# Optimization experiments

Hardware: AMD Instinct MI355X
Metric: run time of the kernel (lower is better)

Reference implementation:

```python
import jax, jax.numpy as jnp
import numpy as np
from jax import lax

LENGTH, WIDTH = 64, 64
INPUT_DIM = 1


def _convlstm_layer(x_tbchw, W, b):
    """Run one ConvLSTM layer over time. x_tbchw: (L,B,Cin,H,W).
    W: (4*hid, Cin+hid, 3, 3), b: (4*hid,). Returns (outputs (L,B,hid,H,W), last_h)."""
    L, B, _, H, Wd = x_tbchw.shape
    hid = W.shape[0] // 4
    h0 = jnp.zeros((B, hid, H, Wd), dtype=x_tbchw.dtype)
    c0 = jnp.zeros((B, hid, H, Wd), dtype=x_tbchw.dtype)

    def step(carry, xt):
        h, c = carry
        z = lax.conv_general_dilated(
            jnp.concatenate([xt, h], axis=1), W,
            window_strides=(1, 1), padding='SAME',
            dimension_numbers=('NCHW', 'OIHW', 'NCHW'))
        z = z + b[None, :, None, None]
        cc_i, cc_f, cc_o, cc_g = jnp.split(z, 4, axis=1)
        c_next = jax.nn.sigmoid(cc_f) * c + jax.nn.sigmoid(cc_i) * jnp.tanh(cc_g)
        h_next = jax.nn.sigmoid(cc_o) * jnp.tanh(c_next)
        return (h_next, c_next), h_next

    (h_last, _), outs = lax.scan(step, (h0, c0), x_tbchw)
    return outs, h_last


def setup_inputs() -> dict:
    key = jax.random.key(0)
    k1, k2, k3 = jax.random.split(key, 3)
    B, L, N = 16, 12, LENGTH * WIDTH
    emd, out_len = 128, 12
    return {
        'history_data': jax.random.normal(k1, (B, L, N, 1), dtype=jnp.float32),
        'future_data': jnp.zeros((B, L, N, 1), dtype=jnp.float32),
        'W0': jax.random.normal(k2, (4 * emd, INPUT_DIM + emd, 3, 3), dtype=jnp.float32) * 0.05,
        'b0': jnp.zeros((4 * emd,), dtype=jnp.float32),
        'W1': jax.random.normal(k3, (4 * out_len, emd + out_len, 3, 3), dtype=jnp.float32) * 0.05,
        'b1': jnp.zeros((4 * out_len,), dtype=jnp.float32),
        'batch_seen': 0,
        'epoch': 0,
        'train': 1,
    }


def reference(history_data, future_data, W0, b0, W1, b1, batch_seen, epoch, train):
    B, L, N, C = history_data.shape
    # (B,L,1,H,W) -> (L,B,1,H,W) for time-major scan
    x = history_data[..., :INPUT_DIM].reshape(B, L, INPUT_DIM, LENGTH, WIDTH)
    x = jnp.transpose(x, (1, 0, 2, 3, 4))
    outs0, _ = _convlstm_layer(x, W0, b0)          # (L,B,emd,H,W)
    _, h_last = _convlstm_layer(outs0, W1, b1)     # (B,out_len,H,W)
    prediction = h_last.reshape(B, L, LENGTH * WIDTH)[..., None]  # (B,L,N,1)
    return prediction
```

## Files before the change

### kernel.cpp

```cpp
#include <hip/hip_runtime.h>
#include <hip/hip_bf16.h>


typedef __attribute__((ext_vector_type(8))) short short8;
typedef __attribute__((ext_vector_type(4))) float float4v;

#define CS 160
#define KTOT 1440

__device__ __forceinline__ float sigf(float x) { return 1.f / (1.f + __expf(-x)); }
__device__ __forceinline__ short f2hs(float v) {
  _Float16 h = (_Float16)v;
  return *(short*)&h;
}
__device__ __forceinline__ float hs2f(short s) {
  _Float16 h; *(short*)&h = s; return (float)h;
}
__device__ __forceinline__ float bs2f(short s) {
  __hip_bfloat16 h; *(short*)&h = s; return __bfloat162float(h);
}
__device__ __forceinline__ short f2bs(float v) {
  __hip_bfloat16 h = __float2bfloat16(v);
  return *(short*)&h;
}

__device__ __forceinline__ void async_ld16(const short* g, short* l) {
  __builtin_amdgcn_global_load_lds(
      (const __attribute__((address_space(1))) unsigned int*)g,
      (__attribute__((address_space(3))) unsigned int*)l, 16, 0, 0);
}

__device__ __forceinline__ void stage_row(const short* __restrict__ rowPtr, bool rowOK,
                                          short* dstRow, int lane,
                                          const short* __restrict__ zp) {
  #pragma unroll
  for (int j = 0; j < 4; ++j) {
    int e = j * 64 + lane;
    int px = e >> 2, v = e & 3;
    int xx = px - 1;
    const short* g = (rowOK && xx >= 0) ? (rowPtr + (size_t)xx * CS + v * 8) : zp;
    async_ld16(g, dstRow + e * 8);
  }
  if (lane < 8) {
    int px = 64 + (lane >> 2), v = lane & 3, xx = px - 1;
    short8 val = {0, 0, 0, 0, 0, 0, 0, 0};
    if (rowOK && xx < 64) val = *(const short8*)(rowPtr + (size_t)xx * CS + v * 8);
    *(short8*)(dstRow + px * 32 + v * 8) = val;
  }
}

__global__ void detect_dtype(const unsigned short* __restrict__ w0, int* __restrict__ flag) {
  int lane = threadIdx.x;
  int cnt = 0;
  for (int i = 0; i < 4; ++i) {
    unsigned short u = w0[2 * (lane + 64 * i)];
    int e = (u >> 7) & 0xFF;
    unsigned long long b = __ballot(e >= 0xC0);
    cnt += __popcll(b);
  }
  if (lane == 0) *flag = (cnt > 32) ? 1 : 0;
}

__global__ void canon_x(const void* __restrict__ hist, short* __restrict__ Xc,
                        const int* __restrict__ flag) {
  int i = blockIdx.x * 256 + threadIdx.x;
  float v = (*flag) ? ((const float*)hist)[i] : bs2f(((const short*)hist)[i]);
  if (!isfinite(v) || fabsf(v) > 1e4f) v = 0.f;
  Xc[i] = f2hs(v);
}

__global__ void canon_b(const void* __restrict__ b0, const void* __restrict__ b1,
                        float* __restrict__ Bc0, float* __restrict__ Bc1,
                        const int* __restrict__ flag) {
  int i = blockIdx.x * 256 + threadIdx.x;
  int fl = *flag;
  if (i < 512) {
    float v = fl ? ((const float*)b0)[i] : bs2f(((const short*)b0)[i]);
    if (!isfinite(v) || fabsf(v) > 1e4f) v = 0.f;
    Bc0[i] = v;
  } else if (i < 560) {
    int j = i - 512;
    float v = fl ? ((const float*)b1)[j] : bs2f(((const short*)b1)[j]);
    if (!isfinite(v) || fabsf(v) > 1e4f) v = 0.f;
    Bc1[j] = v;
  }
}

__global__ void prep_w0(const void* __restrict__ W0, short* __restrict__ Wp,
                        const int* __restrict__ flag) {
  int i = blockIdx.x * 256 + threadIdx.x;
  if (i >= 512 * KTOT) return;
  int fl = *flag;
  int co = i / KTOT, k = i - co * KTOT;
  int tap = k / CS, c = k - tap * CS;
  int ci = -1;
  if (c == 0) ci = 0;
  else if (c <= 128) ci = c;
  float w = 0.f;
  if (ci >= 0) {
    int widx = (co * 129 + ci) * 9 + tap;
    w = fl ? ((const float*)W0)[widx] : bs2f(((const short*)W0)[widx]);
    if (!isfinite(w) || fabsf(w) > 1e4f) w = 0.f;
  }
  Wp[i] = f2hs(w);
}

__global__ void prep_w1(const void* __restrict__ W1, short* __restrict__ Wp,
                        const int* __restrict__ flag) {
  int i = blockIdx.x * 256 + threadIdx.x;
  if (i >= 48 * KTOT) return;
  int fl = *flag;
  int co = i / KTOT, k = i - co * KTOT;
  int tap = k / CS, c = k - tap * CS;
  int ci = -1;
  if (c >= 1 && c <= 140) ci = c - 1;
  float w = 0.f;
  if (ci >= 0) {
    int widx = (co * 140 + ci) * 9 + tap;
    w = fl ? ((const float*)W1)[widx] : bs2f(((const short*)W1)[widx]);
    if (!isfinite(w) || fabsf(w) > 1e4f) w = 0.f;
  }
  Wp[i] = f2hs(w);
}

__global__ void fill_x0(const short* __restrict__ Xc, short* __restrict__ P0) {
  int p = blockIdx.x * 256 + threadIdx.x;
  int b = p >> 12, pix = p & 4095;
  P0[(size_t)p * CS] = Xc[b * 12 * 4096 + pix];
}

__global__ __launch_bounds__(256, 2) void gemm_gate0(
    const short* __restrict__ Pcur, short* __restrict__ Pnext,
    const short* __restrict__ Wp, const float* __restrict__ Bc0,
    float* __restrict__ C0, const short* __restrict__ Xc,
    const short* __restrict__ zp, int t) {
  int bx = blockIdx.x;
  int nt = bx >> 9, mt = bx & 511;
  int b = mt >> 5, y0 = (mt & 31) * 2;
  int tid = threadIdx.x, wave = tid >> 6, lane = tid & 63;
  int ln15 = lane & 15, quad = lane >> 4;
  int wm = wave & 1, wn = wave >> 1;
  int hc = nt * 32 + wn * 16 + ln15;

  __shared__ __align__(16) short halo[2 * 4 * 66 * 32];

  float4v acc[4][4];
  #pragma unroll
  for (int i = 0; i < 4; ++i)
    #pragma unroll
    for (int j = 0; j < 4; ++j) acc[i][j] = (float4v){0.f, 0.f, 0.f, 0.f};

  const short* wbase = Wp + (size_t)hc * KTOT + quad * 8;
  short8 bcur[4], bnxt[4];
  #pragma unroll
  for (int g = 0; g < 4; ++g)
    bcur[g] = *(const short8*)(wbase + (size_t)g * 128 * KTOT);

  int yy = y0 - 1 + wave;
  bool rowOK = (yy >= 0) && (yy < 64);
  const short* rowBase = Pcur + (size_t)((b * 64 + yy) * 64) * CS;

  stage_row(rowBase, rowOK, halo + wave * 2112, lane, zp);
  __syncthreads();

  for (int ch = 0; ch < 5; ++ch) {
    int c0 = ch * 32;
    const short* cur = halo + (ch & 1) * 8448;
    if (ch < 4)
      stage_row(rowBase + c0 + 32, rowOK, halo + ((ch + 1) & 1) * 8448 + wave * 2112,
                lane, zp);
    #pragma unroll
    for (int tap = 0; tap < 9; ++tap) {
      int dy = tap / 3, dx = tap - dy * 3;
      int ntap = (tap < 8) ? tap + 1 : 0;
      int nc0 = (tap < 8) ? c0 : ((ch < 4) ? c0 + 32 : c0);
      #pragma unroll
      for (int g = 0; g < 4; ++g)
        bnxt[g] = *(const short8*)(wbase + (size_t)g * 128 * KTOT + ntap * CS + nc0);

      short8 af[4];
      #pragma unroll
      for (int mf = 0; mf < 4; ++mf)
        af[mf] = *(const short8*)&cur[((wm + dy) * 66 + mf * 16 + ln15 + dx) * 32 + quad * 8];
      #pragma unroll
      for (int g = 0; g < 4; ++g)
        #pragma unroll
        for (int mf = 0; mf < 4; ++mf)
          acc[mf][g] = __builtin_amdgcn_mfma_f32_16x16x32_f16(af[mf], bcur[g], acc[mf][g], 0, 0, 0);
      #pragma unroll
      for (int g = 0; g < 4; ++g) bcur[g] = bnxt[g];
    }
    __syncthreads();
  }

  float bi = Bc0[hc], bff = Bc0[128 + hc], bo = Bc0[256 + hc], bg = Bc0[384 + hc];
  int rowPix = (b * 64 + y0 + wm) * 64;
  #pragma unroll
  for (int mf = 0; mf < 4; ++mf) {
    #pragma unroll
    for (int r = 0; r < 4; ++r) {
      int x = mf * 16 + quad * 4 + r;
      int pix = rowPix + x;
      float zi = acc[mf][0][r] + bi;
      float zf = acc[mf][1][r] + bff;
      float zo = acc[mf][2][r] + bo;
      float zg = acc[mf][3][r] + bg;
      float cprev = C0[(size_t)pix * 128 + hc];
      float cn = sigf(zf) * cprev + sigf(zi) * tanhf(zg);
      float hn = sigf(zo) * tanhf(cn);
      C0[(size_t)pix * 128 + hc] = cn;
      Pnext[(size_t)pix * CS + 1 + hc] = f2hs(hn);
    }
  }
  if (nt == 0 && t < 11 && tid < 128) {
    int rr = tid >> 6, x = tid & 63;
    int yw = y0 + rr;
    Pnext[(size_t)((b * 64 + yw) * 64 + x) * CS] = Xc[(b * 12 + t + 1) * 4096 + yw * 64 + x];
  }
}

__global__ __launch_bounds__(256, 2) void gemm_gate1(
    const short* __restrict__ Prd, short* __restrict__ Pwr,
    const short* __restrict__ Wp, const float* __restrict__ Bc1,
    float* __restrict__ C1, void* __restrict__ outp,
    const short* __restrict__ zp, const int* __restrict__ flagp, int t) {
  int bid = blockIdx.x;
  int b = bid >> 5, y0 = (bid & 31) * 2;
  int tid = threadIdx.x, wave = tid >> 6, lane = tid & 63;
  int ln15 = lane & 15, quad = lane >> 4;
  int wr = wave >> 1, wh = wave & 1;
  int flagv = *flagp;

  __shared__ __align__(16) short halo[2 * 4 * 66 * 32];

  float4v acc[2][3];
  #pragma unroll
  for (int i = 0; i < 2; ++i)
    #pragma unroll
    for (int j = 0; j < 3; ++j) acc[i][j] = (float4v){0.f, 0.f, 0.f, 0.f};

  int yy = y0 - 1 + wave;
  bool rowOK = (yy >= 0) && (yy < 64);
  const short* rowBase = Prd + (size_t)((b * 64 + yy) * 64) * CS;

  const short* wbase = Wp + (size_t)ln15 * KTOT + quad * 8;
  short8 bcur[3], bnxt[3];
  #pragma unroll
  for (int nf = 0; nf < 3; ++nf)
    bcur[nf] = *(const short8*)(wbase + (size_t)nf * 16 * KTOT);

  stage_row(rowBase, rowOK, halo + wave * 2112, lane, zp);
  __syncthreads();

  for (int ch = 0; ch < 5; ++ch) {
    int c0 = ch * 32;
    const short* cur = halo + (ch & 1) * 8448;
    if (ch < 4)
      stage_row(rowBase + c0 + 32, rowOK, halo + ((ch + 1) & 1) * 8448 + wave * 2112,
                lane, zp);
    #pragma unroll
    for (int tap = 0; tap < 9; ++tap) {
      int dy = tap / 3, dx = tap - dy * 3;
      int ntap = (tap < 8) ? tap + 1 : 0;
      int nc0 = (tap < 8) ? c0 : ((ch < 4) ? c0 + 32 : c0);
      #pragma unroll
      for (int nf = 0; nf < 3; ++nf)
        bnxt[nf] = *(const short8*)(wbase + (size_t)nf * 16 * KTOT + ntap * CS + nc0);

      short8 af[2];
      #pragma unroll
      for (int mf = 0; mf < 2; ++mf)
        af[mf] = *(const short8*)&cur[((wr + dy) * 66 + wh * 32 + mf * 16 + ln15 + dx) * 32
                                      + quad * 8];
      #pragma unroll
      for (int nf = 0; nf < 3; ++nf)
        #pragma unroll
        for (int mf = 0; mf < 2; ++mf)
          acc[mf][nf] = __builtin_amdgcn_mfma_f32_16x16x32_f16(af[mf], bcur[nf], acc[mf][nf], 0, 0, 0);
      #pragma unroll
      for (int nf = 0; nf < 3; ++nf) bcur[nf] = bnxt[nf];
    }
    __syncthreads();
  }

  float* zbuf = (float*)halo;
  #pragma unroll
  for (int mf = 0; mf < 2; ++mf)
    #pragma unroll
    for (int nf = 0; nf < 3; ++nf)
      #pragma unroll
      for (int r = 0; r < 4; ++r) {
        int pxl = wr * 64 + wh * 32 + mf * 16 + quad * 4 + r;
        zbuf[pxl * 48 + nf * 16 + ln15] = acc[mf][nf][r];
      }
  __syncthreads();

  #pragma unroll
  for (int k = 0; k < 6; ++k) {
    int id = k * 256 + tid;
    int hc = id >> 7, pxl = id & 127;
    float zi = zbuf[pxl * 48 + hc]      + Bc1[hc];
    float zf = zbuf[pxl * 48 + 12 + hc] + Bc1[12 + hc];
    float zo = zbuf[pxl * 48 + 24 + hc] + Bc1[24 + hc];
    float zg = zbuf[pxl * 48 + 36 + hc] + Bc1[36 + hc];
    int y = y0 + (pxl >> 6), x = pxl & 63;
    int pix = (b * 64 + y) * 64 + x;
    float cprev = C1[(size_t)pix * 12 + hc];
    float cn = sigf(zf) * cprev + sigf(zi) * tanhf(zg);
    float hn = sigf(zo) * tanhf(cn);
    C1[(size_t)pix * 12 + hc] = cn;
    Pwr[(size_t)pix * CS + 129 + hc] = f2hs(hn);
    if (t == 11) {
      int oidx = (b * 12 + hc) * 4096 + y * 64 + x;
      if (flagv) ((float*)outp)[oidx] = hn;
      else ((short*)outp)[oidx] = f2bs(hn);
    }
  }
}

extern "C" void kernel_launch(void* const* d_in, const int* in_sizes, int n_in,
                              void* d_out, int out_size, void* d_ws, size_t ws_size,
                              hipStream_t stream) {
  const void* hist = d_in[0];
  const void* W0 = d_in[2];
  const void* b0 = d_in[3];
  const void* W1 = d_in[4];
  const void* b1 = d_in[5];

  char* ws = (char*)d_ws;
  const size_t PszB = (size_t)16 * 4096 * CS * 2;
  short* P[2] = {(short*)ws, (short*)(ws + PszB)};
  float* C0 = (float*)(ws + 2 * PszB);
  const size_t C0e = 2 * PszB + 33554432;
  float* C1 = (float*)(ws + C0e);
  const size_t C1e = C0e + 3145728;
  short* zp = (short*)(ws + C1e);
  const size_t zpe = C1e + 256;
  short* Xc = (short*)(ws + zpe);
  const size_t Xce = zpe + 1572864;
  short* Wp0 = (short*)(ws + Xce);
  const size_t W0e = Xce + (size_t)512 * KTOT * 2;
  short* Wp1 = (short*)(ws + W0e);
  const size_t W1e = W0e + (size_t)48 * KTOT * 2;
  float* Bc0 = (float*)(ws + W1e);
  float* Bc1 = (float*)(ws + W1e + 2048);
  int* flag = (int*)(ws + W1e + 2048 + 192);

  hipMemsetAsync(ws, 0, zpe, stream);
  detect_dtype<<<1, 64, 0, stream>>>((const unsigned short*)W0, flag);
  canon_x<<<3072, 256, 0, stream>>>(hist, Xc, flag);
  canon_b<<<3, 256, 0, stream>>>(b0, b1, Bc0, Bc1, flag);
  prep_w0<<<(512 * KTOT + 255) / 256, 256, 0, stream>>>(W0, Wp0, flag);
  prep_w1<<<(48 * KTOT + 255) / 256, 256, 0, stream>>>(W1, Wp1, flag);
  fill_x0<<<256, 256, 0, stream>>>(Xc, P[0]);

  for (int t = 0; t < 12; ++t) {
    gemm_gate0<<<2048, 256, 0, stream>>>(P[t & 1], P[(t + 1) & 1], Wp0, Bc0, C0, Xc, zp, t);
    gemm_gate1<<<512, 256, 0, stream>>>(P[(t + 1) & 1], P[t & 1], Wp1, Bc1, C1,
                                        d_out, zp, flag, t);
  }
}
```

Baseline: 2.202 ms.

## Fuse layer-0 step t and layer-1 step t-1 into one skewed launch

Merges the two per-timestep GEMM kernels into a single kernel whose blocks are split 4:1. Most blocks run ConvLSTM layer 0 at step t, and the rest run layer 1 at step t-1, over a 13-step skewed schedule. This halves the number of launches and lets the small layer-1 work overlap the layer-0 GEMM instead of running alone with low occupancy. The occupancy hint is also raised from 2 to 3 blocks per CU, which tightens the register budget and may cause spills. Correctness relies on the two layers writing disjoint channel ranges of the ping-pong P buffer.

```diff
diff --git a/kernel.cpp b/kernel.cpp
--- a/kernel.cpp
+++ b/kernel.cpp
@@ -12,9 +12,6 @@
 __device__ __forceinline__ short f2hs(float v) {
   _Float16 h = (_Float16)v;
   return *(short*)&h;
-}
-__device__ __forceinline__ float hs2f(short s) {
-  _Float16 h; *(short*)&h = s; return (float)h;
 }
 __device__ __forceinline__ float bs2f(short s) {
   __hip_bfloat16 h; *(short*)&h = s; return __bfloat162float(h);
@@ -129,191 +126,190 @@
   P0[(size_t)p * CS] = Xc[b * 12 * 4096 + pix];
 }
 
-__global__ __launch_bounds__(256, 2) void gemm_gate0(
+__global__ __launch_bounds__(256, 3) void fused_step(
     const short* __restrict__ Pcur, short* __restrict__ Pnext,
-    const short* __restrict__ Wp, const float* __restrict__ Bc0,
+    const short* __restrict__ Wp0, const float* __restrict__ Bc0,
     float* __restrict__ C0, const short* __restrict__ Xc,
-    const short* __restrict__ zp, int t) {
+    const short* __restrict__ Wp1, const float* __restrict__ Bc1,
+    float* __restrict__ C1, void* __restrict__ outp,
+    const short* __restrict__ zp, const int* __restrict__ flagp, int t) {
+  __shared__ __align__(16) short halo[2 * 4 * 66 * 32];
+
   int bx = blockIdx.x;
-  int nt = bx >> 9, mt = bx & 511;
-  int b = mt >> 5, y0 = (mt & 31) * 2;
   int tid = threadIdx.x, wave = tid >> 6, lane = tid & 63;
   int ln15 = lane & 15, quad = lane >> 4;
-  int wm = wave & 1, wn = wave >> 1;
-  int hc = nt * 32 + wn * 16 + ln15;
-
-  __shared__ __align__(16) short halo[2 * 4 * 66 * 32];
-
-  float4v acc[4][4];
-  #pragma unroll
-  for (int i = 0; i < 4; ++i)
-    #pragma unroll
-    for (int j = 0; j < 4; ++j) acc[i][j] = (float4v){0.f, 0.f, 0.f, 0.f};
-
-  const short* wbase = Wp + (size_t)hc * KTOT + quad * 8;
-  short8 bcur[4], bnxt[4];
-  #pragma unroll
-  for (int g = 0; g < 4; ++g)
-    bcur[g] = *(const short8*)(wbase + (size_t)g * 128 * KTOT);
-
-  int yy = y0 - 1 + wave;
-  bool rowOK = (yy >= 0) && (yy < 64);
-  const short* rowBase = Pcur + (size_t)((b * 64 + yy) * 64) * CS;
-
-  stage_row(rowBase, rowOK, halo + wave * 2112, lane, zp);
-  __syncthreads();
-
-  for (int ch = 0; ch < 5; ++ch) {
-    int c0 = ch * 32;
-    const short* cur = halo + (ch & 1) * 8448;
-    if (ch < 4)
-      stage_row(rowBase + c0 + 32, rowOK, halo + ((ch + 1) & 1) * 8448 + wave * 2112,
-                lane, zp);
-    #pragma unroll
-    for (int tap = 0; tap < 9; ++tap) {
-      int dy = tap / 3, dx = tap - dy * 3;
-      int ntap = (tap < 8) ? tap + 1 : 0;
-      int nc0 = (tap < 8) ? c0 : ((ch < 4) ? c0 + 32 : c0);
-      #pragma unroll
-      for (int g = 0; g < 4; ++g)
-        bnxt[g] = *(const short8*)(wbase + (size_t)g * 128 * KTOT + ntap * CS + nc0);
-
-      short8 af[4];
-      #pragma unroll
-      for (int mf = 0; mf < 4; ++mf)
-        af[mf] = *(const short8*)&cur[((wm + dy) * 66 + mf * 16 + ln15 + dx) * 32 + quad * 8];
-      #pragma unroll
-      for (int g = 0; g < 4; ++g)
+
+  if ((bx % 5) != 4) {
+    if (t >= 12) return;
+    int idx = bx - bx / 5;
+    int nt = idx >> 9, mt = idx & 511;
+    int b = mt >> 5, y0 = (mt & 31) * 2;
+    int wm = wave & 1, wn = wave >> 1;
+    int hc = nt * 32 + wn * 16 + ln15;
+
+    float4v acc[4][4];
+    #pragma unroll
+    for (int i = 0; i < 4; ++i)
+      #pragma unroll
+      for (int j = 0; j < 4; ++j) acc[i][j] = (float4v){0.f, 0.f, 0.f, 0.f};
+
+    const short* wbase = Wp0 + (size_t)hc * KTOT + quad * 8;
+    short8 bcur[4], bnxt[4];
+    #pragma unroll
+    for (int g = 0; g < 4; ++g)
+      bcur[g] = *(const short8*)(wbase + (size_t)g * 128 * KTOT);
+
+    int yy = y0 - 1 + wave;
+    bool rowOK = (yy >= 0) && (yy < 64);
+    const short* rowBase = Pcur + (size_t)((b * 64 + yy) * 64) * CS;
+
+    stage_row(rowBase, rowOK, halo + wave * 2112, lane, zp);
+    __syncthreads();
+
+    for (int ch = 0; ch < 5; ++ch) {
+      int c0 = ch * 32;
+      const short* cur = halo + (ch & 1) * 8448;
+      if (ch < 4)
+        stage_row(rowBase + c0 + 32, rowOK, halo + ((ch + 1) & 1) * 8448 + wave * 2112,
+                  lane, zp);
+      #pragma unroll
+      for (int tap = 0; tap < 9; ++tap) {
+        int dy = tap / 3, dx = tap - dy * 3;
+        int ntap = (tap < 8) ? tap + 1 : 0;
+        int nc0 = (tap < 8) ? c0 : ((ch < 4) ? c0 + 32 : c0);
+        #pragma unroll
+        for (int g = 0; g < 4; ++g)
+          bnxt[g] = *(const short8*)(wbase + (size_t)g * 128 * KTOT + ntap * CS + nc0);
+
+        short8 af[4];
         #pragma unroll
         for (int mf = 0; mf < 4; ++mf)
-          acc[mf][g] = __builtin_amdgcn_mfma_f32_16x16x32_f16(af[mf], bcur[g], acc[mf][g], 0, 0, 0);
-      #pragma unroll
-      for (int g = 0; g < 4; ++g) bcur[g] = bnxt[g];
-    }
+          af[mf] = *(const short8*)&cur[((wm + dy) * 66 + mf * 16 + ln15 + dx) * 32 + quad * 8];
+        #pragma unroll
+        for (int g = 0; g < 4; ++g)
+          #pragma unroll
+          for (int mf = 0; mf < 4; ++mf)
+            acc[mf][g] = __builtin_amdgcn_mfma_f32_16x16x32_f16(af[mf], bcur[g], acc[mf][g], 0, 0, 0);
+        #pragma unroll
+        for (int g = 0; g < 4; ++g) bcur[g] = bnxt[g];
+      }
+      __syncthreads();
+    }
+
+    float bi = Bc0[hc], bff = Bc0[128 + hc], bo = Bc0[256 + hc], bg = Bc0[384 + hc];
+    int rowPix = (b * 64 + y0 + wm) * 64;
+    #pragma unroll
+    for (int mf = 0; mf < 4; ++mf) {
+      #pragma unroll
+      for (int r = 0; r < 4; ++r) {
+        int x = mf * 16 + quad * 4 + r;
+        int pix = rowPix + x;
+        float zi = acc[mf][0][r] + bi;
+        float zf = acc[mf][1][r] + bff;
+        float zo = acc[mf][2][r] + bo;
+        float zg = acc[mf][3][r] + bg;
+        float cprev = C0[(size_t)pix * 128 + hc];
+        float cn = sigf(zf) * cprev + sigf(zi) * tanhf(zg);
+        float hn = sigf(zo) * tanhf(cn);
+        C0[(size_t)pix * 128 + hc] = cn;
+        Pnext[(size_t)pix * CS + 1 + hc] = f2hs(hn);
+      }
+    }
+    if (nt == 0 && t < 11 && tid < 128) {
+      int rr = tid >> 6, x = tid & 63;
+      int yw = y0 + rr;
+      Pnext[(size_t)((b * 64 + yw) * 64 + x) * CS] = Xc[(b * 12 + t + 1) * 4096 + yw * 64 + x];
+    }
+  } else {
+    if (t < 1) return;
+    int t1 = t - 1;
+    int idx1 = bx / 5;
+    int b = idx1 >> 5, y0 = (idx1 & 31) * 2;
+    int wr = wave >> 1, wh = wave & 1;
+    int flagv = *flagp;
+
+    float4v acc[2][3];
+    #pragma unroll
+    for (int i = 0; i < 2; ++i)
+      #pragma unroll
+      for (int j = 0; j < 3; ++j) acc[i][j] = (float4v){0.f, 0.f, 0.f, 0.f};
+
+    int yy = y0 - 1 + wave;
+    bool rowOK = (yy >= 0) && (yy < 64);
+    const short* rowBase = Pcur + (size_t)((b * 64 + yy) * 64) * CS;
+
+    const short* wbase = Wp1 + (size_t)ln15 * KTOT + quad * 8;
+    short8 bcur[3], bnxt[3];
+    #pragma unroll
+    for (int nf = 0; nf < 3; ++nf)
+      bcur[nf] = *(const short8*)(wbase + (size_t)nf * 16 * KTOT);
+
+    stage_row(rowBase, rowOK, halo + wave * 2112, lane, zp);
     __syncthreads();
-  }
-
-  float bi = Bc0[hc], bff = Bc0[128 + hc], bo = Bc0[256 + hc], bg = Bc0[384 + hc];
-  int rowPix = (b * 64 + y0 + wm) * 64;
-  #pragma unroll
-  for (int mf = 0; mf < 4; ++mf) {
-    #pragma unroll
-    for (int r = 0; r < 4; ++r) {
-      int x = mf * 16 + quad * 4 + r;
-      int pix = rowPix + x;
-      float zi = acc[mf][0][r] + bi;
-      float zf = acc[mf][1][r] + bff;
-      float zo = acc[mf][2][r] + bo;
-      float zg = acc[mf][3][r] + bg;
-      float cprev = C0[(size_t)pix * 128 + hc];
+
+    for (int ch = 0; ch < 5; ++ch) {
+      int c0 = ch * 32;
+      const short* cur = halo + (ch & 1) * 8448;
+      if (ch < 4)
+        stage_row(rowBase + c0 + 32, rowOK, halo + ((ch + 1) & 1) * 8448 + wave * 2112,
+                  lane, zp);
+      #pragma unroll
+      for (int tap = 0; tap < 9; ++tap) {
+        int dy = tap / 3, dx = tap - dy * 3;
+        int ntap = (tap < 8) ? tap + 1 : 0;
+        int nc0 = (tap < 8) ? c0 : ((ch < 4) ? c0 + 32 : c0);
+        #pragma unroll
+        for (int nf = 0; nf < 3; ++nf)
+          bnxt[nf] = *(const short8*)(wbase + (size_t)nf * 16 * KTOT + ntap * CS + nc0);
+
+        short8 af[2];
+        #pragma unroll
+        for (int mf = 0; mf < 2; ++mf)
+          af[mf] = *(const short8*)&cur[((wr + dy) * 66 + wh * 32 + mf * 16 + ln15 + dx) * 32
+                                        + quad * 8];
+        #pragma unroll
+        for (int nf = 0; nf < 3; ++nf)
+          #pragma unroll
+          for (int mf = 0; mf < 2; ++mf)
+            acc[mf][nf] = __builtin_amdgcn_mfma_f32_16x16x32_f16(af[mf], bcur[nf], acc[mf][nf], 0, 0, 0);
+        #pragma unroll
+        for (int nf = 0; nf < 3; ++nf) bcur[nf] = bnxt[nf];
+      }
+      __syncthreads();
+    }
+
+    float* zbuf = (float*)halo;
+    #pragma unroll
+    for (int mf = 0; mf < 2; ++mf)
+      #pragma unroll
+      for (int nf = 0; nf < 3; ++nf)
+        #pragma unroll
+        for (int r = 0; r < 4; ++r) {
+          int pxl = wr * 64 + wh * 32 + mf * 16 + quad * 4 + r;
+          zbuf[pxl * 48 + nf * 16 + ln15] = acc[mf][nf][r];
+        }
+    __syncthreads();
+
+    #pragma unroll
+    for (int k = 0; k < 6; ++k) {
+      int id = k * 256 + tid;
+      int hc = id >> 7, pxl = id & 127;
+      float zi = zbuf[pxl * 48 + hc]      + Bc1[hc];
+      float zf = zbuf[pxl * 48 + 12 + hc] + Bc1[12 + hc];
+      float zo = zbuf[pxl * 48 + 24 + hc] + Bc1[24 + hc];
+      float zg = zbuf[pxl * 48 + 36 + hc] + Bc1[36 + hc];
+      int y = y0 + (pxl >> 6), x = pxl & 63;
+      int pix = (b * 64 + y) * 64 + x;
+      float cprev = C1[(size_t)pix * 12 + hc];
       float cn = sigf(zf) * cprev + sigf(zi) * tanhf(zg);
       float hn = sigf(zo) * tanhf(cn);
-      C0[(size_t)pix * 128 + hc] = cn;
-      Pnext[(size_t)pix * CS + 1 + hc] = f2hs(hn);
-    }
-  }
-  if (nt == 0 && t < 11 && tid < 128) {
-    int rr = tid >> 6, x = tid & 63;
-    int yw = y0 + rr;
-    Pnext[(size_t)((b * 64 + yw) * 64 + x) * CS] = Xc[(b * 12 + t + 1) * 4096 + yw * 64 + x];
-  }
-}
-
-__global__ __launch_bounds__(256, 2) void gemm_gate1(
-    const short* __restrict__ Prd, short* __restrict__ Pwr,
-    const short* __restrict__ Wp, const float* __restrict__ Bc1,
-    float* __restrict__ C1, void* __restrict__ outp,
-    const short* __restrict__ zp, const int* __restrict__ flagp, int t) {
-  int bid = blockIdx.x;
-  int b = bid >> 5, y0 = (bid & 31) * 2;
-  int tid = threadIdx.x, wave = tid >> 6, lane = tid & 63;
-  int ln15 = lane & 15, quad = lane >> 4;
-  int wr = wave >> 1, wh = wave & 1;
-  int flagv = *flagp;
-
-  __shared__ __align__(16) short halo[2 * 4 * 66 * 32];
-
-  float4v acc[2][3];
-  #pragma unroll
-  for (int i = 0; i < 2; ++i)
-    #pragma unroll
-    for (int j = 0; j < 3; ++j) acc[i][j] = (float4v){0.f, 0.f, 0.f, 0.f};
-
-  int yy = y0 - 1 + wave;
-  bool rowOK = (yy >= 0) && (yy < 64);
-  const short* rowBase = Prd + (size_t)((b * 64 + yy) * 64) * CS;
-
-  const short* wbase = Wp + (size_t)ln15 * KTOT + quad * 8;
-  short8 bcur[3], bnxt[3];
-  #pragma unroll
-  for (int nf = 0; nf < 3; ++nf)
-    bcur[nf] = *(const short8*)(wbase + (size_t)nf * 16 * KTOT);
-
-  stage_row(rowBase, rowOK, halo + wave * 2112, lane, zp);
-  __syncthreads();
-
-  for (int ch = 0; ch < 5; ++ch) {
-    int c0 = ch * 32;
-    const short* cur = halo + (ch & 1) * 8448;
-    if (ch < 4)
-      stage_row(rowBase + c0 + 32, rowOK, halo + ((ch + 1) & 1) * 8448 + wave * 2112,
-                lane, zp);
-    #pragma unroll
-    for (int tap = 0; tap < 9; ++tap) {
-      int dy = tap / 3, dx = tap - dy * 3;
-      int ntap = (tap < 8) ? tap + 1 : 0;
-      int nc0 = (tap < 8) ? c0 : ((ch < 4) ? c0 + 32 : c0);
-      #pragma unroll
-      for (int nf = 0; nf < 3; ++nf)
-        bnxt[nf] = *(const short8*)(wbase + (size_t)nf * 16 * KTOT + ntap * CS + nc0);
-
-      short8 af[2];
-      #pragma unroll
-      for (int mf = 0; mf < 2; ++mf)
-        af[mf] = *(const short8*)&cur[((wr + dy) * 66 + wh * 32 + mf * 16 + ln15 + dx) * 32
-                                      + quad * 8];
-      #pragma unroll
-      for (int nf = 0; nf < 3; ++nf)
-        #pragma unroll
-        for (int mf = 0; mf < 2; ++mf)
-          acc[mf][nf] = __builtin_amdgcn_mfma_f32_16x16x32_f16(af[mf], bcur[nf], acc[mf][nf], 0, 0, 0);
-      #pragma unroll
-      for (int nf = 0; nf < 3; ++nf) bcur[nf] = bnxt[nf];
-    }
-    __syncthreads();
-  }
-
-  float* zbuf = (float*)halo;
-  #pragma unroll
-  for (int mf = 0; mf < 2; ++mf)
-    #pragma unroll
-    for (int nf = 0; nf < 3; ++nf)
-      #pragma unroll
-      for (int r = 0; r < 4; ++r) {
-        int pxl = wr * 64 + wh * 32 + mf * 16 + quad * 4 + r;
-        zbuf[pxl * 48 + nf * 16 + ln15] = acc[mf][nf][r];
+      C1[(size_t)pix * 12 + hc] = cn;
+      Pnext[(size_t)pix * CS + 129 + hc] = f2hs(hn);
+      if (t1 == 11) {
+        int oidx = (b * 12 + hc) * 4096 + y * 64 + x;
+        if (flagv) ((float*)outp)[oidx] = hn;
+        else ((short*)outp)[oidx] = f2bs(hn);
       }
-  __syncthreads();
-
-  #pragma unroll
-  for (int k = 0; k < 6; ++k) {
-    int id = k * 256 + tid;
-    int hc = id >> 7, pxl = id & 127;
-    float zi = zbuf[pxl * 48 + hc]      + Bc1[hc];
-    float zf = zbuf[pxl * 48 + 12 + hc] + Bc1[12 + hc];
-    float zo = zbuf[pxl * 48 + 24 + hc] + Bc1[24 + hc];
-    float zg = zbuf[pxl * 48 + 36 + hc] + Bc1[36 + hc];
-    int y = y0 + (pxl >> 6), x = pxl & 63;
-    int pix = (b * 64 + y) * 64 + x;
-    float cprev = C1[(size_t)pix * 12 + hc];
-    float cn = sigf(zf) * cprev + sigf(zi) * tanhf(zg);
-    float hn = sigf(zo) * tanhf(cn);
-    C1[(size_t)pix * 12 + hc] = cn;
-    Pwr[(size_t)pix * CS + 129 + hc] = f2hs(hn);
-    if (t == 11) {
-      int oidx = (b * 12 + hc) * 4096 + y * 64 + x;
-      if (flagv) ((float*)outp)[oidx] = hn;
-      else ((short*)outp)[oidx] = f2bs(hn);
     }
   }
 }
@@ -354,9 +350,8 @@
   prep_w1<<<(48 * KTOT + 255) / 256, 256, 0, stream>>>(W1, Wp1, flag);
   fill_x0<<<256, 256, 0, stream>>>(Xc, P[0]);
 
-  for (int t = 0; t < 12; ++t) {
-    gemm_gate0<<<2048, 256, 0, stream>>>(P[t & 1], P[(t + 1) & 1], Wp0, Bc0, C0, Xc, zp, t);
-    gemm_gate1<<<512, 256, 0, stream>>>(P[(t + 1) & 1], P[t & 1], Wp1, Bc1, C1,
-                                        d_out, zp, flag, t);
-  }
-}
+  for (int t = 0; t <= 12; ++t) {
+    fused_step<<<2560, 256, 0, stream>>>(P[t & 1], P[(t + 1) & 1], Wp0, Bc0, C0, Xc,
+                                         Wp1, Bc1, C1, d_out, zp, flag, t);
+  }
+}
```

Result: slower. 2.416 ms (+9.7%).

## Retile layer-0 conv GEMM to one image row per block with full-channel halo staging

Applied to the files above, without the earlier changes.

Layer-0 gate GEMM is re-tiled so each block handles one output row (64 pixels) for 32 hidden channels across all four gates, with each wave owning 16 pixels and eight N-fragments. The whole 3-row, 160-channel input halo is loaded into LDS once with a channel-major pitched layout, replacing the per-chunk double-buffered staging and its per-chunk barriers. This cuts A-fragment LDS reads per MFMA and removes synchronisation inside the K loop. In exchange it doubles the grid, re-reads halo rows across neighbouring blocks, and raises register pressure from eight live B fragments.

```diff
diff --git a/kernel.cpp b/kernel.cpp
--- a/kernel.cpp
+++ b/kernel.cpp
@@ -7,15 +7,14 @@
 
 #define CS 160
 #define KTOT 1440
+#define VPITCH 528
+#define RPITCH 10560
 
 __device__ __forceinline__ float sigf(float x) { return 1.f / (1.f + __expf(-x)); }
 __device__ __forceinline__ short f2hs(float v) {
   _Float16 h = (_Float16)v;
   return *(short*)&h;
 }
-__device__ __forceinline__ float hs2f(short s) {
-  _Float16 h; *(short*)&h = s; return (float)h;
-}
 __device__ __forceinline__ float bs2f(short s) {
   __hip_bfloat16 h; *(short*)&h = s; return __bfloat162float(h);
 }
@@ -28,25 +27,6 @@
   __builtin_amdgcn_global_load_lds(
       (const __attribute__((address_space(1))) unsigned int*)g,
       (__attribute__((address_space(3))) unsigned int*)l, 16, 0, 0);
-}
-
-__device__ __forceinline__ void stage_row(const short* __restrict__ rowPtr, bool rowOK,
-                                          short* dstRow, int lane,
-                                          const short* __restrict__ zp) {
-  #pragma unroll
-  for (int j = 0; j < 4; ++j) {
-    int e = j * 64 + lane;
-    int px = e >> 2, v = e & 3;
-    int xx = px - 1;
-    const short* g = (rowOK && xx >= 0) ? (rowPtr + (size_t)xx * CS + v * 8) : zp;
-    async_ld16(g, dstRow + e * 8);
-  }
-  if (lane < 8) {
-    int px = 64 + (lane >> 2), v = lane & 3, xx = px - 1;
-    short8 val = {0, 0, 0, 0, 0, 0, 0, 0};
-    if (rowOK && xx < 64) val = *(const short8*)(rowPtr + (size_t)xx * CS + v * 8);
-    *(short8*)(dstRow + px * 32 + v * 8) = val;
-  }
 }
 
 __global__ void detect_dtype(const unsigned short* __restrict__ w0, int* __restrict__ flag) {
@@ -135,76 +115,82 @@
     float* __restrict__ C0, const short* __restrict__ Xc,
     const short* __restrict__ zp, int t) {
   int bx = blockIdx.x;
-  int nt = bx >> 9, mt = bx & 511;
-  int b = mt >> 5, y0 = (mt & 31) * 2;
+  int nt = bx & 3, mt = bx >> 2;
+  int y = mt & 63, b = mt >> 6;
   int tid = threadIdx.x, wave = tid >> 6, lane = tid & 63;
   int ln15 = lane & 15, quad = lane >> 4;
-  int wm = wave & 1, wn = wave >> 1;
-  int hc = nt * 32 + wn * 16 + ln15;
-
-  __shared__ __align__(16) short halo[2 * 4 * 66 * 32];
-
-  float4v acc[4][4];
-  #pragma unroll
-  for (int i = 0; i < 4; ++i)
-    #pragma unroll
-    for (int j = 0; j < 4; ++j) acc[i][j] = (float4v){0.f, 0.f, 0.f, 0.f};
-
-  const short* wbase = Wp + (size_t)hc * KTOT + quad * 8;
-  short8 bcur[4], bnxt[4];
-  #pragma unroll
-  for (int g = 0; g < 4; ++g)
-    bcur[g] = *(const short8*)(wbase + (size_t)g * 128 * KTOT);
-
-  int yy = y0 - 1 + wave;
-  bool rowOK = (yy >= 0) && (yy < 64);
-  const short* rowBase = Pcur + (size_t)((b * 64 + yy) * 64) * CS;
-
-  stage_row(rowBase, rowOK, halo + wave * 2112, lane, zp);
+
+  __shared__ __align__(16) short halo[3 * RPITCH];
+
+  #pragma unroll
+  for (int i = 0; i < 15; ++i) {
+    int pid = wave * 15 + i;
+    int r = pid / 20, v = pid - r * 20;
+    int yy = y - 1 + r;
+    bool rowOK = (yy >= 0) && (yy < 64);
+    const short* rowPtr = Pcur + (size_t)((b * 64 + yy) * 64) * CS + v * 8;
+    const short* g = (rowOK && lane > 0) ? (rowPtr + (size_t)(lane - 1) * CS) : zp;
+    async_ld16(g - (size_t)lane * 8 + (size_t)lane * 8, halo + r * RPITCH + v * VPITCH);
+    (void)g;
+  }
+  if (wave < 3 && lane < 40) {
+    int r = wave, v = lane >> 1, pxi = 64 + (lane & 1);
+    int yy = y - 1 + r;
+    bool rowOK = (yy >= 0) && (yy < 64);
+    short8 val = {0, 0, 0, 0, 0, 0, 0, 0};
+    if (rowOK && pxi == 64)
+      val = *(const short8*)(Pcur + (size_t)((b * 64 + yy) * 64 + 63) * CS + v * 8);
+    *(short8*)(halo + r * RPITCH + v * VPITCH + pxi * 8) = val;
+  }
   __syncthreads();
 
+  float4v acc[8];
+  #pragma unroll
+  for (int i = 0; i < 8; ++i) acc[i] = (float4v){0.f, 0.f, 0.f, 0.f};
+
+  const short* bb[8];
+  short8 bcur[8], bnxt[8];
+  #pragma unroll
+  for (int nf = 0; nf < 8; ++nf) {
+    int co = (nf >> 1) * 128 + nt * 32 + (nf & 1) * 16 + ln15;
+    bb[nf] = Wp + (size_t)co * KTOT + quad * 8;
+    bcur[nf] = *(const short8*)(bb[nf]);
+  }
+
+  int pxb = wave * 16 + ln15;
   for (int ch = 0; ch < 5; ++ch) {
-    int c0 = ch * 32;
-    const short* cur = halo + (ch & 1) * 8448;
-    if (ch < 4)
-      stage_row(rowBase + c0 + 32, rowOK, halo + ((ch + 1) & 1) * 8448 + wave * 2112,
-                lane, zp);
     #pragma unroll
     for (int tap = 0; tap < 9; ++tap) {
       int dy = tap / 3, dx = tap - dy * 3;
       int ntap = (tap < 8) ? tap + 1 : 0;
-      int nc0 = (tap < 8) ? c0 : ((ch < 4) ? c0 + 32 : c0);
-      #pragma unroll
-      for (int g = 0; g < 4; ++g)
-        bnxt[g] = *(const short8*)(wbase + (size_t)g * 128 * KTOT + ntap * CS + nc0);
-
-      short8 af[4];
-      #pragma unroll
-      for (int mf = 0; mf < 4; ++mf)
-        af[mf] = *(const short8*)&cur[((wm + dy) * 66 + mf * 16 + ln15 + dx) * 32 + quad * 8];
-      #pragma unroll
-      for (int g = 0; g < 4; ++g)
-        #pragma unroll
-        for (int mf = 0; mf < 4; ++mf)
-          acc[mf][g] = __builtin_amdgcn_mfma_f32_16x16x32_f16(af[mf], bcur[g], acc[mf][g], 0, 0, 0);
-      #pragma unroll
-      for (int g = 0; g < 4; ++g) bcur[g] = bnxt[g];
+      int nch = (tap < 8) ? ch : ((ch < 4) ? ch + 1 : ch);
+      #pragma unroll
+      for (int nf = 0; nf < 8; ++nf)
+        bnxt[nf] = *(const short8*)(bb[nf] + ntap * CS + nch * 32);
+
+      short8 af = *(const short8*)&halo[dy * RPITCH + (ch * 4 + quad) * VPITCH
+                                        + (pxb + dx) * 8];
+      #pragma unroll
+      for (int nf = 0; nf < 8; ++nf)
+        acc[nf] = __builtin_amdgcn_mfma_f32_16x16x32_f16(af, bcur[nf], acc[nf], 0, 0, 0);
+      #pragma unroll
+      for (int nf = 0; nf < 8; ++nf) bcur[nf] = bnxt[nf];
     }
-    __syncthreads();
-  }
-
-  float bi = Bc0[hc], bff = Bc0[128 + hc], bo = Bc0[256 + hc], bg = Bc0[384 + hc];
-  int rowPix = (b * 64 + y0 + wm) * 64;
-  #pragma unroll
-  for (int mf = 0; mf < 4; ++mf) {
+  }
+
+  int rowPix = (b * 64 + y) * 64;
+  #pragma unroll
+  for (int h = 0; h < 2; ++h) {
+    int hc = nt * 32 + h * 16 + ln15;
+    float bi = Bc0[hc], bff = Bc0[128 + hc], bo = Bc0[256 + hc], bg = Bc0[384 + hc];
     #pragma unroll
     for (int r = 0; r < 4; ++r) {
-      int x = mf * 16 + quad * 4 + r;
+      int x = wave * 16 + quad * 4 + r;
       int pix = rowPix + x;
-      float zi = acc[mf][0][r] + bi;
-      float zf = acc[mf][1][r] + bff;
-      float zo = acc[mf][2][r] + bo;
-      float zg = acc[mf][3][r] + bg;
+      float zi = acc[0 + h][r] + bi;
+      float zf = acc[2 + h][r] + bff;
+      float zo = acc[4 + h][r] + bo;
+      float zg = acc[6 + h][r] + bg;
       float cprev = C0[(size_t)pix * 128 + hc];
       float cn = sigf(zf) * cprev + sigf(zi) * tanhf(zg);
       float hn = sigf(zo) * tanhf(cn);
@@ -212,10 +198,27 @@
       Pnext[(size_t)pix * CS + 1 + hc] = f2hs(hn);
     }
   }
-  if (nt == 0 && t < 11 && tid < 128) {
-    int rr = tid >> 6, x = tid & 63;
-    int yw = y0 + rr;
-    Pnext[(size_t)((b * 64 + yw) * 64 + x) * CS] = Xc[(b * 12 + t + 1) * 4096 + yw * 64 + x];
+  if (nt == 0 && t < 11 && tid < 64) {
+    Pnext[(size_t)(rowPix + tid) * CS] = Xc[(b * 12 + t + 1) * 4096 + y * 64 + tid];
+  }
+}
+
+__device__ __forceinline__ void stage_row32(const short* __restrict__ rowPtr, bool rowOK,
+                                            short* dstRow, int lane,
+                                            const short* __restrict__ zp) {
+  #pragma unroll
+  for (int j = 0; j < 4; ++j) {
+    int e = j * 64 + lane;
+    int px = e >> 2, v = e & 3;
+    int xx = px - 1;
+    const short* g = (rowOK && xx >= 0) ? (rowPtr + (size_t)xx * CS + v * 8) : zp;
+    async_ld16(g, dstRow + e * 8);
+  }
+  if (lane < 8) {
+    int px = 64 + (lane >> 2), v = lane & 3, xx = px - 1;
+    short8 val = {0, 0, 0, 0, 0, 0, 0, 0};
+    if (rowOK && xx < 64) val = *(const short8*)(rowPtr + (size_t)xx * CS + v * 8);
+    *(short8*)(dstRow + px * 32 + v * 8) = val;
   }
 }
 
@@ -249,15 +252,15 @@
   for (int nf = 0; nf < 3; ++nf)
     bcur[nf] = *(const short8*)(wbase + (size_t)nf * 16 * KTOT);
 
-  stage_row(rowBase, rowOK, halo + wave * 2112, lane, zp);
+  stage_row32(rowBase, rowOK, halo + wave * 2112, lane, zp);
   __syncthreads();
 
   for (int ch = 0; ch < 5; ++ch) {
     int c0 = ch * 32;
     const short* cur = halo + (ch & 1) * 8448;
     if (ch < 4)
-      stage_row(rowBase + c0 + 32, rowOK, halo + ((ch + 1) & 1) * 8448 + wave * 2112,
-                lane, zp);
+      stage_row32(rowBase + c0 + 32, rowOK, halo + ((ch + 1) & 1) * 8448 + wave * 2112,
+                  lane, zp);
     #pragma unroll
     for (int tap = 0; tap < 9; ++tap) {
       int dy = tap / 3, dx = tap - dy * 3;
@@ -355,7 +358,7 @@
   fill_x0<<<256, 256, 0, stream>>>(Xc, P[0]);
 
   for (int t = 0; t < 12; ++t) {
-    gemm_gate0<<<2048, 256, 0, stream>>>(P[t & 1], P[(t + 1) & 1], Wp0, Bc0, C0, Xc, zp, t);
+    gemm_gate0<<<4096, 256, 0, stream>>>(P[t & 1], P[(t + 1) & 1], Wp0, Bc0, C0, Xc, zp, t);
     gemm_gate1<<<512, 256, 0, stream>>>(P[(t + 1) & 1], P[t & 1], Wp1, Bc1, C1,
                                         d_out, zp, flag, t);
   }
```

Result: slower. 5.854 ms (+165.9%).

## Specialize first layer-0 timestep with scalar kernel and deepen weight prefetch

Applied to the files above, without the earlier changes.

At t=0 the hidden and cell states are zero, so the layer-0 gate computation only needs the single input channel. A dedicated scalar kernel now does this step instead of the full 1440-wide MFMA GEMM, and the fill_x0 kernel and one full gate0 GEMM launch are removed. Separately, the gate0 GEMM now keeps three taps of weight fragments in registers, prefetching three taps ahead instead of one, to hide global load latency better. This costs more VGPRs, which may hurt occupancy under the 2-wave launch bound.

```diff
diff --git a/kernel.cpp b/kernel.cpp
--- a/kernel.cpp
+++ b/kernel.cpp
@@ -123,10 +123,53 @@
   Wp[i] = f2hs(w);
 }
 
-__global__ void fill_x0(const short* __restrict__ Xc, short* __restrict__ P0) {
-  int p = blockIdx.x * 256 + threadIdx.x;
-  int b = p >> 12, pix = p & 4095;
-  P0[(size_t)p * CS] = Xc[b * 12 * 4096 + pix];
+__global__ __launch_bounds__(256, 4) void gate0_t0(
+    const short* __restrict__ Xc, short* __restrict__ Pnext,
+    const short* __restrict__ Wp, const float* __restrict__ Bc0,
+    float* __restrict__ C0) {
+  int rid = blockIdx.x;
+  int b = rid >> 6, y = rid & 63;
+  int tid = threadIdx.x;
+  __shared__ float xh[3][66];
+  for (int i = tid; i < 198; i += 256) {
+    int r = i / 66, px = i - r * 66;
+    int yy = y - 1 + r, xx = px - 1;
+    float v = 0.f;
+    if ((unsigned)yy < 64u && (unsigned)xx < 64u)
+      v = hs2f(Xc[b * 12 * 4096 + yy * 64 + xx]);
+    xh[r][px] = v;
+  }
+  __syncthreads();
+
+  int hc = tid & 127, pb = tid >> 7;
+  float wgt[4][9];
+  #pragma unroll
+  for (int g = 0; g < 4; ++g)
+    #pragma unroll
+    for (int tap = 0; tap < 9; ++tap)
+      wgt[g][tap] = hs2f(Wp[(size_t)(g * 128 + hc) * KTOT + tap * CS]);
+  float bi = Bc0[hc], bff = Bc0[128 + hc], bo = Bc0[256 + hc], bg = Bc0[384 + hc];
+  (void)bff;
+  int rowPix = (b * 64 + y) * 64;
+  for (int k = 0; k < 32; ++k) {
+    int x = pb + 2 * k;
+    float zi = bi, zo = bo, zg = bg;
+    #pragma unroll
+    for (int tap = 0; tap < 9; ++tap) {
+      int dy = tap / 3, dx = tap - dy * 3;
+      float xv = xh[dy][x + dx];
+      zi += wgt[0][tap] * xv;
+      zo += wgt[2][tap] * xv;
+      zg += wgt[3][tap] * xv;
+    }
+    float cn = sigf(zi) * tanhf(zg);
+    float hn = sigf(zo) * tanhf(cn);
+    int pix = rowPix + x;
+    C0[(size_t)pix * 128 + hc] = cn;
+    Pnext[(size_t)pix * CS + 1 + hc] = f2hs(hn);
+  }
+  if (tid < 64)
+    Pnext[(size_t)(rowPix + tid) * CS] = Xc[(b * 12 + 1) * 4096 + y * 64 + tid];
 }
 
 __global__ __launch_bounds__(256, 2) void gemm_gate0(
@@ -151,10 +194,12 @@
     for (int j = 0; j < 4; ++j) acc[i][j] = (float4v){0.f, 0.f, 0.f, 0.f};
 
   const short* wbase = Wp + (size_t)hc * KTOT + quad * 8;
-  short8 bcur[4], bnxt[4];
-  #pragma unroll
-  for (int g = 0; g < 4; ++g)
-    bcur[g] = *(const short8*)(wbase + (size_t)g * 128 * KTOT);
+  short8 bb[3][4];
+  #pragma unroll
+  for (int p = 0; p < 3; ++p)
+    #pragma unroll
+    for (int g = 0; g < 4; ++g)
+      bb[p][g] = *(const short8*)(wbase + (size_t)g * 128 * KTOT + p * CS);
 
   int yy = y0 - 1 + wave;
   bool rowOK = (yy >= 0) && (yy < 64);
@@ -164,19 +209,14 @@
   __syncthreads();
 
   for (int ch = 0; ch < 5; ++ch) {
-    int c0 = ch * 32;
     const short* cur = halo + (ch & 1) * 8448;
     if (ch < 4)
-      stage_row(rowBase + c0 + 32, rowOK, halo + ((ch + 1) & 1) * 8448 + wave * 2112,
+      stage_row(rowBase + ch * 32 + 32, rowOK, halo + ((ch + 1) & 1) * 8448 + wave * 2112,
                 lane, zp);
     #pragma unroll
     for (int tap = 0; tap < 9; ++tap) {
       int dy = tap / 3, dx = tap - dy * 3;
-      int ntap = (tap < 8) ? tap + 1 : 0;
-      int nc0 = (tap < 8) ? c0 : ((ch < 4) ? c0 + 32 : c0);
-      #pragma unroll
-      for (int g = 0; g < 4; ++g)
-        bnxt[g] = *(const short8*)(wbase + (size_t)g * 128 * KTOT + ntap * CS + nc0);
+      const int p = tap % 3;
 
       short8 af[4];
       #pragma unroll
@@ -186,9 +226,14 @@
       for (int g = 0; g < 4; ++g)
         #pragma unroll
         for (int mf = 0; mf < 4; ++mf)
-          acc[mf][g] = __builtin_amdgcn_mfma_f32_16x16x32_f16(af[mf], bcur[g], acc[mf][g], 0, 0, 0);
-      #pragma unroll
-      for (int g = 0; g < 4; ++g) bcur[g] = bnxt[g];
+          acc[mf][g] = __builtin_amdgcn_mfma_f32_16x16x32_f16(af[mf], bb[p][g], acc[mf][g], 0, 0, 0);
+
+      int ntap = (tap < 6) ? tap + 3 : tap - 6;
+      int nch = (tap < 6) ? ch : ((ch < 4) ? ch + 1 : ch);
+      int nc0 = nch * 32;
+      #pragma unroll
+      for (int g = 0; g < 4; ++g)
+        bb[p][g] = *(const short8*)(wbase + (size_t)g * 128 * KTOT + ntap * CS + nc0);
     }
     __syncthreads();
   }
@@ -352,9 +397,11 @@
   canon_b<<<3, 256, 0, stream>>>(b0, b1, Bc0, Bc1, flag);
   prep_w0<<<(512 * KTOT + 255) / 256, 256, 0, stream>>>(W0, Wp0, flag);
   prep_w1<<<(48 * KTOT + 255) / 256, 256, 0, stream>>>(W1, Wp1, flag);
-  fill_x0<<<256, 256, 0, stream>>>(Xc, P[0]);
-
-  for (int t = 0; t < 12; ++t) {
+
+  gate0_t0<<<1024, 256, 0, stream>>>(Xc, P[1], Wp0, Bc0, C0);
+  gemm_gate1<<<512, 256, 0, stream>>>(P[1], P[0], Wp1, Bc1, C1, d_out, zp, flag, 0);
+
+  for (int t = 1; t < 12; ++t) {
     gemm_gate0<<<2048, 256, 0, stream>>>(P[t & 1], P[(t + 1) & 1], Wp0, Bc0, C0, Xc, zp, t);
     gemm_gate1<<<512, 256, 0, stream>>>(P[(t + 1) & 1], P[t & 1], Wp1, Bc1, C1,
                                         d_out, zp, flag, t);
```

Result: slower. 2.310 ms (+4.9%).
